# Kernel optimization log

Hardware: AMD Instinct MI355X
Metric: run time of the kernel (lower is better)

## Reference

```python
import jax, jax.numpy as jnp
import numpy as np

HEADS = 8
EPS = 1e-5
PW1 = (512, 8, 14, 14)   # (C, T, H, W), C = headsize1 * heads
PW2 = (512, 32, 7, 7)


def _ln(x, g, b):
    m = jnp.mean(x, axis=-1, keepdims=True)
    v = jnp.var(x, axis=-1, keepdims=True)
    return (x - m) * jax.lax.rsqrt(v + EPS) * g + b


def _mha(q, k, v):
    b, nq, c = q.shape
    nk = k.shape[1]
    hd = c // HEADS
    qh = q.reshape(b, nq, HEADS, hd).transpose(0, 2, 1, 3)  # [b,h,nq,hd]
    kh = k.reshape(b, nk, HEADS, hd).transpose(0, 2, 1, 3)
    vh = v.reshape(b, nk, HEADS, hd).transpose(0, 2, 1, 3)
    s = jnp.einsum('bhqd,bhkd->bhqk', qh, kh) * (hd ** -0.5)
    a = jax.nn.softmax(s, axis=-1)
    o = jnp.einsum('bhqk,bhkd->bhqd', a, vh)
    return o.transpose(0, 2, 1, 3).reshape(b, nq, c)


def _tok(x):
    b, c, t, h, w = x.shape
    return x.transpose(0, 2, 3, 4, 1).reshape(b, t * h * w, c)


def _detok(t, c, T, H, W):
    b = t.shape[0]
    return t.reshape(b, T, H, W, c).transpose(0, 4, 1, 2, 3)


def _out_head(y, w, bias, bn_g, bn_b):
    # 1x1x1 Conv3d + ReLU + BatchNorm3d (eval, running mean 0 / var 1)
    z = jnp.einsum('bcthw,oc->bothw', y, w) + bias[None, :, None, None, None]
    z = jax.nn.relu(z)
    z = z * jax.lax.rsqrt(jnp.float32(1.0 + EPS))
    return z * bn_g[None, :, None, None, None] + bn_b[None, :, None, None, None]


def reference(x1, x2, Wq1, bq1, Wk1, bk1, Wv1, bv1, ln1_g, ln1_b,
              Wq2, bq2, Wk2, bk2, Wv2, bv2, ln2_g, ln2_b,
              out1_w, out1_b, bn1_g, bn1_b, out2_w, out2_b, bn2_g, bn2_b):
    t1 = _tok(x1)  # [B, 1568, 512]
    t2 = _tok(x2)  # [B, 1568, 512]
    for i in range(3):  # three chained norm + cross-attn stages
        q1 = _ln(t1, ln1_g[i], ln1_b[i]) @ Wq1[i].T + bq1[i]
        k1 = t2 @ Wk1[i].T + bk1[i]
        v1 = t2 @ Wv1[i].T + bv1[i]
        q2 = _ln(t2, ln2_g[i], ln2_b[i]) @ Wq2[i].T + bq2[i]
        k2 = t1 @ Wk2[i].T + bk2[i]
        v2 = t1 @ Wv2[i].T + bv2[i]
        t1 = t1 + _mha(q1, k1, v1)
        t2 = t2 + _mha(q2, k2, v2)
    y1 = _detok(t1, *PW1)
    y2 = _detok(t2, *PW2)
    z1 = _out_head(y1, out1_w, out1_b, bn1_g, bn1_b)
    z2 = _out_head(y2, out2_w, out2_b, bn2_g, bn2_b)
    return (z1, z2)


def setup_inputs() -> dict:
    key = jax.random.key(0)
    ks = jax.random.split(key, 12)
    C = 512
    w = lambda k, shp: jax.random.normal(k, shp, jnp.float32) * 0.02
    return {
        'x1': jax.random.normal(ks[0], (4, C, 8, 14, 14), jnp.float32),
        'x2': jax.random.normal(ks[1], (4, C, 32, 7, 7), jnp.float32),
        'Wq1': w(ks[2], (3, C, C)), 'bq1': jnp.zeros((3, C), jnp.float32),
        'Wk1': w(ks[3], (3, C, C)), 'bk1': jnp.zeros((3, C), jnp.float32),
        'Wv1': w(ks[4], (3, C, C)), 'bv1': jnp.zeros((3, C), jnp.float32),
        'ln1_g': jnp.ones((3, C), jnp.float32), 'ln1_b': jnp.zeros((3, C), jnp.float32),
        'Wq2': w(ks[5], (3, C, C)), 'bq2': jnp.zeros((3, C), jnp.float32),
        'Wk2': w(ks[6], (3, C, C)), 'bk2': jnp.zeros((3, C), jnp.float32),
        'Wv2': w(ks[7], (3, C, C)), 'bv2': jnp.zeros((3, C), jnp.float32),
        'ln2_g': jnp.ones((3, C), jnp.float32), 'ln2_b': jnp.zeros((3, C), jnp.float32),
        'out1_w': w(ks[8], (C, C)), 'out1_b': jnp.zeros((C,), jnp.float32),
        'bn1_g': jnp.ones((C,), jnp.float32), 'bn1_b': jnp.zeros((C,), jnp.float32),
        'out2_w': w(ks[9], (C, C)), 'out2_b': jnp.zeros((C,), jnp.float32),
        'bn2_g': jnp.ones((C,), jnp.float32), 'bn2_b': jnp.zeros((C,), jnp.float32),
    }
```

## Files before the change

kernel.cpp:

```cpp
#include <hip/hip_runtime.h>

typedef __bf16 bf16_t;
typedef __bf16 bf16x8 __attribute__((ext_vector_type(8)));
typedef __bf16 bf16x4 __attribute__((ext_vector_type(4)));
typedef float f32x4 __attribute__((ext_vector_type(4)));
typedef float f32x16 __attribute__((ext_vector_type(16)));
typedef unsigned u32x4 __attribute__((ext_vector_type(4)));

#define NTOK 1568
#define CDIM 512
#define BATCH 4
#define MROWS (BATCH*NTOK)
#define RSQ1PEPS 0.9999950000374997f
#define CEXP 0.1803368801111204f

__device__ __forceinline__ float fexp2(float x) {
  float r;
  asm("v_exp_f32 %0, %1" : "=v"(r) : "v"(x));
  return r;
}

__device__ __forceinline__ void glds16(const bf16_t* src, bf16_t* dst) {
  __builtin_amdgcn_global_load_lds(
      (const __attribute__((address_space(1))) unsigned*)src,
      (__attribute__((address_space(3))) unsigned*)dst, 16, 0, 0);
}

struct CastArgs { const float* s[20]; };
__global__ __launch_bounds__(256) void cast_kernel(CastArgs ca, bf16_t* __restrict__ out) {
  int idx = blockIdx.x * 256 + threadIdx.x;
  int m = idx >> 16;
  const float4* sp = (const float4*)ca.s[m];
  float4 v = sp[idx & 65535];
  bf16x4 o;
  o[0] = (bf16_t)v.x; o[1] = (bf16_t)v.y; o[2] = (bf16_t)v.z; o[3] = (bf16_t)v.w;
  *(bf16x4*)(out + (size_t)idx * 4) = o;
}

struct TokArgs { const float* x[2]; float* tf[2]; bf16_t* tb[2]; };
__global__ __launch_bounds__(256) void tok_kernel(TokArgs ta) {
  __shared__ float tile[32][33];
  int z = blockIdx.z, sel = z >> 2, b = z & 3;
  int c0 = blockIdx.y * 32, s0 = blockIdx.x * 32;
  int tx = threadIdx.x, ty = threadIdx.y;
  const float* xp = ta.x[sel] + (size_t)b * CDIM * NTOK;
  for (int r = 0; r < 32; r += 8)
    tile[ty + r][tx] = xp[(size_t)(c0 + ty + r) * NTOK + s0 + tx];
  __syncthreads();
  float* tfp = ta.tf[sel] + (size_t)b * NTOK * CDIM;
  bf16_t* tbp = ta.tb[sel] + (size_t)b * NTOK * CDIM;
  for (int r = 0; r < 32; r += 8) {
    float v = tile[tx][ty + r];
    size_t idx = (size_t)(s0 + ty + r) * CDIM + c0 + tx;
    tfp[idx] = v;
    tbp[idx] = (bf16_t)v;
  }
}

__global__ __launch_bounds__(64) void ln_kernel(
    const float* __restrict__ t1, const float* __restrict__ t2,
    const float* __restrict__ g1, const float* __restrict__ b1,
    const float* __restrict__ g2, const float* __restrict__ b2,
    bf16_t* __restrict__ o1, bf16_t* __restrict__ o2) {
  int row = blockIdx.x;
  const float* t; const float* g; const float* bt; bf16_t* out;
  if (row < MROWS) { t = t1; g = g1; bt = b1; out = o1; }
  else { row -= MROWS; t = t2; g = g2; bt = b2; out = o2; }
  int l = threadIdx.x;
  const float* x = t + (size_t)row * CDIM;
  float4 v0 = ((const float4*)x)[l];
  float4 v1 = ((const float4*)x)[l + 64];
  float s = v0.x + v0.y + v0.z + v0.w + v1.x + v1.y + v1.z + v1.w;
  float sq = v0.x*v0.x + v0.y*v0.y + v0.z*v0.z + v0.w*v0.w
           + v1.x*v1.x + v1.y*v1.y + v1.z*v1.z + v1.w*v1.w;
  for (int m = 1; m < 64; m <<= 1) { s += __shfl_xor(s, m); sq += __shfl_xor(sq, m); }
  float mean = s * (1.f / 512.f);
  float var = sq * (1.f / 512.f) - mean * mean;
  float rs = rsqrtf(var + 1e-5f);
  float4 g0 = ((const float4*)g)[l], g1v = ((const float4*)g)[l + 64];
  float4 b0 = ((const float4*)bt)[l], b1v = ((const float4*)bt)[l + 64];
  bf16x4 o0, o1v;
  o0[0] = (bf16_t)((v0.x - mean) * rs * g0.x + b0.x);
  o0[1] = (bf16_t)((v0.y - mean) * rs * g0.y + b0.y);
  o0[2] = (bf16_t)((v0.z - mean) * rs * g0.z + b0.z);
  o0[3] = (bf16_t)((v0.w - mean) * rs * g0.w + b0.w);
  o1v[0] = (bf16_t)((v1.x - mean) * rs * g1v.x + b1v.x);
  o1v[1] = (bf16_t)((v1.y - mean) * rs * g1v.y + b1v.y);
  o1v[2] = (bf16_t)((v1.z - mean) * rs * g1v.z + b1v.z);
  o1v[3] = (bf16_t)((v1.w - mean) * rs * g1v.w + b1v.w);
  *(bf16x4*)(out + (size_t)row * CDIM + l * 4) = o0;
  *(bf16x4*)(out + (size_t)row * CDIM + 256 + l * 4) = o1v;
}

template<int MODE>
__device__ __forceinline__ void gemm_core(
    bf16_t (* __restrict__ As)[40], bf16_t (* __restrict__ Bs)[40],
    const bf16_t* __restrict__ A, const bf16_t* __restrict__ Bp,
    const float* __restrict__ bias, const float* __restrict__ bng,
    const float* __restrict__ bnb, bf16_t* __restrict__ outb,
    float* __restrict__ outf, int m0, int n0, int Nvalid, float scl) {
  int tid = threadIdx.x;
  int w = tid >> 6, l = tid & 63, lr = l & 15, kg = l >> 4;
  int wm = (w >> 1) * 64, wn = (w & 1) * 64;
  f32x4 acc[4][4];
  for (int i = 0; i < 4; i++)
    for (int j = 0; j < 4; j++)
      acc[i][j] = f32x4{0.f, 0.f, 0.f, 0.f};
  int srow = tid >> 1;
  int soff = (tid & 1) * 16;
  int brow = n0 + srow;
  if (MODE != 0 && brow >= Nvalid) brow = Nvalid - 1;
  const bf16_t* aq = A + (size_t)(m0 + srow) * CDIM + soff;
  const bf16_t* bq = Bp + (size_t)brow * CDIM + soff;
  for (int kk = 0; kk < 16; kk++) {
    __syncthreads();
    bf16x8 a0 = *(const bf16x8*)(aq);
    bf16x8 a1 = *(const bf16x8*)(aq + 8);
    bf16x8 b0 = *(const bf16x8*)(bq);
    bf16x8 b1 = *(const bf16x8*)(bq + 8);
    aq += 32; bq += 32;
    *(bf16x8*)&As[srow][soff] = a0;
    *(bf16x8*)&As[srow][soff + 8] = a1;
    *(bf16x8*)&Bs[srow][soff] = b0;
    *(bf16x8*)&Bs[srow][soff + 8] = b1;
    __syncthreads();
    bf16x8 af[4], bfr[4];
    for (int i = 0; i < 4; i++) af[i] = *(const bf16x8*)&As[wm + i * 16 + lr][kg * 8];
    for (int j = 0; j < 4; j++) bfr[j] = *(const bf16x8*)&Bs[wn + j * 16 + lr][kg * 8];
    for (int i = 0; i < 4; i++)
      for (int j = 0; j < 4; j++)
        acc[i][j] = __builtin_amdgcn_mfma_f32_16x16x32_bf16(af[i], bfr[j], acc[i][j], 0, 0, 0);
  }
  for (int i = 0; i < 4; i++)
    for (int j = 0; j < 4; j++) {
      int rbase = m0 + wm + i * 16 + kg * 4;
      int col = n0 + wn + j * 16 + lr;
      for (int r = 0; r < 4; r++) {
        int row = rbase + r;
        float v = acc[i][j][r];
        if (MODE == 0) {
          v = (v + bias[col]) * scl;
          outb[(size_t)row * CDIM + col] = (bf16_t)v;
        } else if (MODE == 1) {
          v += bias[row];
          v = v > 0.f ? v : 0.f;
          v *= RSQ1PEPS;
          v = v * bng[row] + bnb[row];
          if (col < Nvalid) outf[(size_t)row * NTOK + col] = v;
        } else {
          v += bias[row];
          if (col < Nvalid) outb[(size_t)row * NTOK + col] = (bf16_t)v;
        }
      }
    }
}

struct ProjArgs {
  const bf16_t* A0[4]; const bf16_t* W0[4]; const float* b0[4]; bf16_t* o0[4];
  float scl0[4];
  const bf16_t* W2[2]; const bf16_t* B2[2]; const float* b2[2]; bf16_t* o2[2];
};
__global__ __launch_bounds__(256) void proj_kernel(ProjArgs p) {
  __shared__ bf16_t As[128][40];
  __shared__ bf16_t Bs[128][40];
  int id = blockIdx.x;
  if (id < 784) {
    int set = id / 196, rem = id % 196;
    int n0 = (rem & 3) * 128, m0 = (rem >> 2) * 128;
    gemm_core<0>(As, Bs, p.A0[set], p.W0[set], p.b0[set], nullptr, nullptr,
                 p.o0[set], nullptr, m0, n0, 512, p.scl0[set]);
  } else {
    int j = id - 784;
    int unit = j / 52;
    int which = unit >> 2, bat = unit & 3;
    int rem = j % 52;
    int n0 = (rem % 13) * 128, m0 = (rem / 13) * 128;
    gemm_core<2>(As, Bs, p.W2[which], p.B2[which] + (size_t)bat * NTOK * CDIM,
                 p.b2[which], nullptr, nullptr,
                 p.o2[which] + (size_t)bat * CDIM * NTOK, nullptr, m0, n0, NTOK, 1.f);
  }
}

__global__ __launch_bounds__(256) void head_kernel(
    const bf16_t* __restrict__ W1, const bf16_t* __restrict__ W2,
    const bf16_t* __restrict__ t1b, const bf16_t* __restrict__ t2b,
    const float* __restrict__ b1, const float* __restrict__ b2,
    const float* __restrict__ bng1, const float* __restrict__ bnb1,
    const float* __restrict__ bng2, const float* __restrict__ bnb2,
    float* __restrict__ out) {
  __shared__ bf16_t As[128][40];
  __shared__ bf16_t Bs[128][40];
  int z = blockIdx.z;
  int which = z >> 2, bat = z & 3;
  const bf16_t* A = which ? W2 : W1;
  const bf16_t* Bp = (which ? t2b : t1b) + (size_t)bat * NTOK * CDIM;
  const float* bias = which ? b2 : b1;
  const float* bng = which ? bng2 : bng1;
  const float* bnb = which ? bnb2 : bnb1;
  float* outf = out + (size_t)which * BATCH * CDIM * NTOK + (size_t)bat * CDIM * NTOK;
  int m0 = blockIdx.y * 128, n0 = blockIdx.x * 128;
  gemm_core<1>(As, Bs, A, Bp, bias, bng, bnb, nullptr, outf, m0, n0, NTOK, 1.f);
}

__device__ __forceinline__ void build_frags(const float* p, bf16x8& Fa, bf16x8& Fb) {
  unsigned pk[8];
#pragma unroll
  for (int g = 0; g < 8; g++) {
    union { bf16_t hh[2]; unsigned u; } cv;
    cv.hh[0] = (bf16_t)p[2 * g];
    cv.hh[1] = (bf16_t)p[2 * g + 1];
    pk[g] = cv.u;
  }
  asm volatile("v_permlane32_swap_b32 %0, %1" : "+v"(pk[0]), "+v"(pk[2]));
  asm volatile("v_permlane32_swap_b32 %0, %1" : "+v"(pk[1]), "+v"(pk[3]));
  asm volatile("v_permlane32_swap_b32 %0, %1" : "+v"(pk[4]), "+v"(pk[6]));
  asm volatile("v_permlane32_swap_b32 %0, %1" : "+v"(pk[5]), "+v"(pk[7]));
  union { u32x4 u; bf16x8 bv; } A, B;
  A.u[0] = pk[0]; A.u[1] = pk[1]; A.u[2] = pk[2]; A.u[3] = pk[3];
  B.u[0] = pk[4]; B.u[1] = pk[5]; B.u[2] = pk[6]; B.u[3] = pk[7];
  Fa = A.bv; Fb = B.bv;
}

struct AttnArgs {
  const bf16_t* q[2]; const bf16_t* k[2]; const bf16_t* v[2];
  float* tf[2]; bf16_t* tb[2];
};

#define STAGE(TN, SL)                                                         \
  {                                                                           \
    int tnS_ = (TN); if (tnS_ > 48) tnS_ = 48;                                \
    glds16(kgl + (size_t)tnS_ * (32 * CDIM), &Ks[SL][wq8][0]);                \
    glds16(vgl + tnS_ * 32, &Vs[SL][wq16][0]);                                \
  }

#define QK(SL, SA)                                                            \
  {                                                                           \
    const bf16_t* kr_ = &Ks[SL][lo][0];                                       \
    __builtin_amdgcn_s_setprio(1);                                            \
    SA = __builtin_amdgcn_mfma_f32_32x32x16_bf16(                             \
        *(const bf16x8*)(kr_ + ((hi * 8) ^ sw3)), qf[0], z, 0, 0, 0);         \
    SA = __builtin_amdgcn_mfma_f32_32x32x16_bf16(                             \
        *(const bf16x8*)(kr_ + ((16 + hi * 8) ^ sw3)), qf[1], SA, 0, 0, 0);   \
    SA = __builtin_amdgcn_mfma_f32_32x32x16_bf16(                             \
        *(const bf16x8*)(kr_ + ((32 + hi * 8) ^ sw3)), qf[2], SA, 0, 0, 0);   \
    SA = __builtin_amdgcn_mfma_f32_32x32x16_bf16(                             \
        *(const bf16x8*)(kr_ + ((48 + hi * 8) ^ sw3)), qf[3], SA, 0, 0, 0);   \
    __builtin_amdgcn_s_setprio(0);                                            \
  }

#define FIN(SA, SL)                                                           \
  {                                                                           \
    float pa_[16];                                                            \
    _Pragma("unroll")                                                         \
    for (int r_ = 0; r_ < 16; r_++) pa_[r_] = fexp2(SA[r_]);                  \
    bf16x8 F0_, F1_;                                                          \
    build_frags(pa_, F0_, F1_);                                               \
    __builtin_amdgcn_s_setprio(1);                                            \
    ls = __builtin_amdgcn_mfma_f32_32x32x16_bf16(kone, F0_, ls, 0, 0, 0);     \
    ls = __builtin_amdgcn_mfma_f32_32x32x16_bf16(kone, F1_, ls, 0, 0, 0);     \
    ot0 = __builtin_amdgcn_mfma_f32_32x32x16_bf16(                            \
        *(const bf16x8*)(&Vs[SL][lo][(hi * 8) ^ sw2]), F0_, ot0, 0, 0, 0);    \
    ot0 = __builtin_amdgcn_mfma_f32_32x32x16_bf16(                            \
        *(const bf16x8*)(&Vs[SL][lo][(16 + hi * 8) ^ sw2]), F1_, ot0, 0, 0, 0);\
    ot1 = __builtin_amdgcn_mfma_f32_32x32x16_bf16(                            \
        *(const bf16x8*)(&Vs[SL][32 + lo][(hi * 8) ^ sw2]), F0_, ot1, 0, 0, 0);\
    ot1 = __builtin_amdgcn_mfma_f32_32x32x16_bf16(                            \
        *(const bf16x8*)(&Vs[SL][32 + lo][(16 + hi * 8) ^ sw2]), F1_, ot1, 0, 0, 0);\
    __builtin_amdgcn_s_setprio(0);                                            \
  }

#define PAIR(T, S0_, S1_, S2_, SS1, SS2)                                      \
  {                                                                           \
    STAGE((T) + 4, SS1);                                                      \
    STAGE((T) + 5, SS2);                                                      \
    QK(S1_, saB);                                                             \
    FIN(saA, S0_);                                                            \
    QK(S2_, saA);                                                             \
    FIN(saB, S1_);                                                            \
    asm volatile("s_waitcnt vmcnt(2)" ::: "memory");                          \
    __builtin_amdgcn_s_barrier();                                             \
  }

__global__ __launch_bounds__(256) void attn_kernel(AttnArgs aa) {
  __shared__ alignas(16) bf16_t Ks[6][32][64];
  __shared__ alignas(16) bf16_t Vs[6][64][32];
  int id = blockIdx.x;
  int xcd = id & 7, sl = id >> 3;
  int g = xcd + ((sl / 13) << 3);
  int qt = sl % 13;
  int ss = g >> 5, b = (g >> 3) & 3, h = g & 7;
  const bf16_t* qg = aa.q[ss];
  const bf16_t* kgp = aa.k[ss];
  const bf16_t* vtg = aa.v[ss];
  float* tf = aa.tf[ss];
  bf16_t* tb = aa.tb[ss];
  int tid = threadIdx.x, w = tid >> 6, l = tid & 63;
  int lo = l & 31, hi = l >> 5;
  int wq8 = w * 8, wq16 = w * 16;
  int sw3 = (lo & 7) << 3;
  int sw2 = ((lo >> 1) & 3) << 3;
  const size_t kbase = ((size_t)b * NTOK) * CDIM + h * 64;
  const size_t vbase = ((size_t)b * CDIM + h * 64) * NTOK;

  int q0 = qt * 128 + w * 32;
  int qrow = q0 + lo;
  int qr = qrow < NTOK ? qrow : NTOK - 1;
  const bf16_t* qp = qg + kbase + (size_t)qr * CDIM + hi * 8;
  bf16x8 qf[4];
  qf[0] = *(const bf16x8*)(qp);
  qf[1] = *(const bf16x8*)(qp + 16);
  qf[2] = *(const bf16x8*)(qp + 32);
  qf[3] = *(const bf16x8*)(qp + 48);
  asm volatile("" : "+v"(qf[0]), "+v"(qf[1]), "+v"(qf[2]), "+v"(qf[3]));
  asm volatile("s_waitcnt vmcnt(0)" ::: "memory");

  const bf16_t* kgl = kgp + kbase + (size_t)(wq8 + (l >> 3)) * CDIM
                      + (((l & 7) ^ ((l >> 3) & 7)) << 3);
  const bf16_t* vgl = vtg + vbase + (size_t)(wq16 + (l >> 2)) * NTOK
                      + (((l & 3) ^ ((l >> 3) & 3)) << 3);

  bf16x8 kone;
#pragma unroll
  for (int j = 0; j < 8; j++) kone[j] = (bf16_t)1.0f;

  f32x16 ot0, ot1, ls, z, saA, saB;
#pragma unroll
  for (int r = 0; r < 16; r++) { ot0[r] = 0.f; ot1[r] = 0.f; ls[r] = 0.f; z[r] = 0.f; }

  STAGE(0, 0);
  STAGE(1, 1);
  STAGE(2, 2);
  STAGE(3, 3);
  asm volatile("s_waitcnt vmcnt(2)" ::: "memory");
  __builtin_amdgcn_s_barrier();
  QK(0, saA);

  for (int t = 0; t <= 42; t += 6) {
    PAIR(t + 0, 0, 1, 2, 4, 5);
    PAIR(t + 2, 2, 3, 4, 0, 1);
    PAIR(t + 4, 4, 5, 0, 2, 3);
  }
  FIN(saA, 0);
  asm volatile("s_waitcnt vmcnt(0)" ::: "memory");

  if (qrow < NTOK) {
    float inv = 1.f / ls[0];
    float* tfp = tf + ((size_t)b * NTOK + qrow) * CDIM + h * 64 + hi * 4;
    bf16_t* tbp = tb + ((size_t)b * NTOK + qrow) * CDIM + h * 64 + hi * 4;
#pragma unroll
    for (int db = 0; db < 2; db++) {
#pragma unroll
      for (int gq = 0; gq < 4; gq++) {
        int doff = db * 32 + gq * 8;
        float4 old = *(float4*)(tfp + doff);
        float4 nv;
        float a0 = (db ? ot1[gq * 4 + 0] : ot0[gq * 4 + 0]) * inv;
        float a1 = (db ? ot1[gq * 4 + 1] : ot0[gq * 4 + 1]) * inv;
        float a2 = (db ? ot1[gq * 4 + 2] : ot0[gq * 4 + 2]) * inv;
        float a3 = (db ? ot1[gq * 4 + 3] : ot0[gq * 4 + 3]) * inv;
        nv.x = old.x + a0; nv.y = old.y + a1; nv.z = old.z + a2; nv.w = old.w + a3;
        *(float4*)(tfp + doff) = nv;
        bf16x4 ob;
        ob[0] = (bf16_t)nv.x; ob[1] = (bf16_t)nv.y;
        ob[2] = (bf16_t)nv.z; ob[3] = (bf16_t)nv.w;
        *(bf16x4*)(tbp + doff) = ob;
      }
    }
  }
}

extern "C" void kernel_launch(void* const* d_in, const int* in_sizes, int n_in,
                              void* d_out, int out_size, void* d_ws, size_t ws_size,
                              hipStream_t stream) {
  (void)in_sizes; (void)n_in; (void)out_size; (void)ws_size;
  const float* x1 = (const float*)d_in[0];
  const float* x2 = (const float*)d_in[1];
  const float* Wq1 = (const float*)d_in[2];
  const float* bq1 = (const float*)d_in[3];
  const float* Wk1 = (const float*)d_in[4];
  const float* bk1 = (const float*)d_in[5];
  const float* Wv1 = (const float*)d_in[6];
  const float* bv1 = (const float*)d_in[7];
  const float* ln1_g = (const float*)d_in[8];
  const float* ln1_b = (const float*)d_in[9];
  const float* Wq2 = (const float*)d_in[10];
  const float* bq2 = (const float*)d_in[11];
  const float* Wk2 = (const float*)d_in[12];
  const float* bk2 = (const float*)d_in[13];
  const float* Wv2 = (const float*)d_in[14];
  const float* bv2 = (const float*)d_in[15];
  const float* ln2_g = (const float*)d_in[16];
  const float* ln2_b = (const float*)d_in[17];
  const float* out1_w = (const float*)d_in[18];
  const float* out1_b = (const float*)d_in[19];
  const float* bn1_g = (const float*)d_in[20];
  const float* bn1_b = (const float*)d_in[21];
  const float* out2_w = (const float*)d_in[22];
  const float* out2_b = (const float*)d_in[23];
  const float* bn2_g = (const float*)d_in[24];
  const float* bn2_b = (const float*)d_in[25];

  const size_t WMAT = 512 * 512;
  char* ws = (char*)d_ws;
  bf16_t* wb = (bf16_t*)ws;
  size_t off = 20 * WMAT * sizeof(bf16_t);
  float* t1f = (float*)(ws + off); off += (size_t)MROWS * CDIM * 4;
  float* t2f = (float*)(ws + off); off += (size_t)MROWS * CDIM * 4;
  bf16_t* t1b = (bf16_t*)(ws + off); off += (size_t)MROWS * CDIM * 2;
  bf16_t* t2b = (bf16_t*)(ws + off); off += (size_t)MROWS * CDIM * 2;
  bf16_t* l1b = (bf16_t*)(ws + off); off += (size_t)MROWS * CDIM * 2;
  bf16_t* l2b = (bf16_t*)(ws + off); off += (size_t)MROWS * CDIM * 2;
  bf16_t* q1b = (bf16_t*)(ws + off); off += (size_t)MROWS * CDIM * 2;
  bf16_t* k1b = (bf16_t*)(ws + off); off += (size_t)MROWS * CDIM * 2;
  bf16_t* v1b = (bf16_t*)(ws + off); off += (size_t)MROWS * CDIM * 2;
  bf16_t* q2b = (bf16_t*)(ws + off); off += (size_t)MROWS * CDIM * 2;
  bf16_t* k2b = (bf16_t*)(ws + off); off += (size_t)MROWS * CDIM * 2;
  bf16_t* v2b = (bf16_t*)(ws + off); off += (size_t)MROWS * CDIM * 2;

  CastArgs ca;
  for (int i = 0; i < 3; i++) {
    ca.s[0 + i] = Wq1 + (size_t)i * WMAT;
    ca.s[3 + i] = Wk1 + (size_t)i * WMAT;
    ca.s[6 + i] = Wv1 + (size_t)i * WMAT;
    ca.s[9 + i] = Wq2 + (size_t)i * WMAT;
    ca.s[12 + i] = Wk2 + (size_t)i * WMAT;
    ca.s[15 + i] = Wv2 + (size_t)i * WMAT;
  }
  ca.s[18] = out1_w;
  ca.s[19] = out2_w;
  cast_kernel<<<5120, 256, 0, stream>>>(ca, wb);

  TokArgs ta;
  ta.x[0] = x1; ta.x[1] = x2;
  ta.tf[0] = t1f; ta.tf[1] = t2f;
  ta.tb[0] = t1b; ta.tb[1] = t2b;
  tok_kernel<<<dim3(49, 16, 8), dim3(32, 8), 0, stream>>>(ta);

  AttnArgs aa;
  aa.q[0] = q1b; aa.q[1] = q2b;
  aa.k[0] = k1b; aa.k[1] = k2b;
  aa.v[0] = v1b; aa.v[1] = v2b;
  aa.tf[0] = t1f; aa.tf[1] = t2f;
  aa.tb[0] = t1b; aa.tb[1] = t2b;

  for (int i = 0; i < 3; i++) {
    ln_kernel<<<2 * MROWS, 64, 0, stream>>>(t1f, t2f,
        ln1_g + i * 512, ln1_b + i * 512, ln2_g + i * 512, ln2_b + i * 512,
        l1b, l2b);
    ProjArgs pa;
    pa.A0[0] = l1b; pa.W0[0] = wb + (0 + i) * WMAT; pa.b0[0] = bq1 + i * 512; pa.o0[0] = q1b;
    pa.A0[1] = t2b; pa.W0[1] = wb + (3 + i) * WMAT; pa.b0[1] = bk1 + i * 512; pa.o0[1] = k1b;
    pa.A0[2] = l2b; pa.W0[2] = wb + (9 + i) * WMAT; pa.b0[2] = bq2 + i * 512; pa.o0[2] = q2b;
    pa.A0[3] = t1b; pa.W0[3] = wb + (12 + i) * WMAT; pa.b0[3] = bk2 + i * 512; pa.o0[3] = k2b;
    pa.scl0[0] = CEXP; pa.scl0[1] = 1.f; pa.scl0[2] = CEXP; pa.scl0[3] = 1.f;
    pa.W2[0] = wb + (6 + i) * WMAT; pa.B2[0] = t2b; pa.b2[0] = bv1 + i * 512; pa.o2[0] = v1b;
    pa.W2[1] = wb + (15 + i) * WMAT; pa.B2[1] = t1b; pa.b2[1] = bv2 + i * 512; pa.o2[1] = v2b;
    proj_kernel<<<1200, 256, 0, stream>>>(pa);
    attn_kernel<<<832, 256, 0, stream>>>(aa);
  }

  float* out = (float*)d_out;
  head_kernel<<<dim3(13, 4, 8), 256, 0, stream>>>(
      wb + 18 * WMAT, wb + 19 * WMAT, t1b, t2b,
      out1_b, out2_b, bn1_g, bn1_b, bn2_g, bn2_b, out);
}
```

Baseline: 394.7 us.

## Double-buffer GEMM tiles with direct global-to-LDS loads and XOR swizzle

```diff
diff --git a/kernel.cpp b/kernel.cpp
--- a/kernel.cpp
+++ b/kernel.cpp
@@ -94,7 +94,7 @@
 
 template<int MODE>
 __device__ __forceinline__ void gemm_core(
-    bf16_t (* __restrict__ As)[40], bf16_t (* __restrict__ Bs)[40],
+    bf16_t (* __restrict__ As)[128][32], bf16_t (* __restrict__ Bs)[128][32],
     const bf16_t* __restrict__ A, const bf16_t* __restrict__ Bp,
     const float* __restrict__ bias, const float* __restrict__ bng,
     const float* __restrict__ bnb, bf16_t* __restrict__ outb,
@@ -106,31 +106,47 @@
   for (int i = 0; i < 4; i++)
     for (int j = 0; j < 4; j++)
       acc[i][j] = f32x4{0.f, 0.f, 0.f, 0.f};
-  int srow = tid >> 1;
-  int soff = (tid & 1) * 16;
-  int brow = n0 + srow;
-  if (MODE != 0 && brow >= Nvalid) brow = Nvalid - 1;
-  const bf16_t* aq = A + (size_t)(m0 + srow) * CDIM + soff;
-  const bf16_t* bq = Bp + (size_t)brow * CDIM + soff;
+
+  int srow = w * 16 + (l >> 2);
+  int scol = ((l & 3) ^ ((l >> 3) & 3)) << 3;
+  const bf16_t* aq0 = A + (size_t)(m0 + srow) * CDIM + scol;
+  const bf16_t* aq1 = aq0 + (size_t)64 * CDIM;
+  int br0 = n0 + srow, br1 = n0 + srow + 64;
+  if (MODE != 0) {
+    if (br0 > Nvalid - 1) br0 = Nvalid - 1;
+    if (br1 > Nvalid - 1) br1 = Nvalid - 1;
+  }
+  const bf16_t* bq0 = Bp + (size_t)br0 * CDIM + scol;
+  const bf16_t* bq1 = Bp + (size_t)br1 * CDIM + scol;
+  int swr = ((lr >> 1) & 3) << 3;
+  int wq = w * 16;
+
+  glds16(aq0, &As[0][wq][0]);
+  glds16(aq1, &As[0][64 + wq][0]);
+  glds16(bq0, &Bs[0][wq][0]);
+  glds16(bq1, &Bs[0][64 + wq][0]);
+  __syncthreads();
+
   for (int kk = 0; kk < 16; kk++) {
-    __syncthreads();
-    bf16x8 a0 = *(const bf16x8*)(aq);
-    bf16x8 a1 = *(const bf16x8*)(aq + 8);
-    bf16x8 b0 = *(const bf16x8*)(bq);
-    bf16x8 b1 = *(const bf16x8*)(bq + 8);
-    aq += 32; bq += 32;
-    *(bf16x8*)&As[srow][soff] = a0;
-    *(bf16x8*)&As[srow][soff + 8] = a1;
-    *(bf16x8*)&Bs[srow][soff] = b0;
-    *(bf16x8*)&Bs[srow][soff + 8] = b1;
-    __syncthreads();
+    int bu = kk & 1;
+    if (kk < 15) {
+      int ko = (kk + 1) * 32;
+      glds16(aq0 + ko, &As[bu ^ 1][wq][0]);
+      glds16(aq1 + ko, &As[bu ^ 1][64 + wq][0]);
+      glds16(bq0 + ko, &Bs[bu ^ 1][wq][0]);
+      glds16(bq1 + ko, &Bs[bu ^ 1][64 + wq][0]);
+    }
     bf16x8 af[4], bfr[4];
-    for (int i = 0; i < 4; i++) af[i] = *(const bf16x8*)&As[wm + i * 16 + lr][kg * 8];
-    for (int j = 0; j < 4; j++) bfr[j] = *(const bf16x8*)&Bs[wn + j * 16 + lr][kg * 8];
+    for (int i = 0; i < 4; i++)
+      af[i] = *(const bf16x8*)&As[bu][wm + i * 16 + lr][(kg * 8) ^ swr];
+    for (int j = 0; j < 4; j++)
+      bfr[j] = *(const bf16x8*)&Bs[bu][wn + j * 16 + lr][(kg * 8) ^ swr];
     for (int i = 0; i < 4; i++)
       for (int j = 0; j < 4; j++)
         acc[i][j] = __builtin_amdgcn_mfma_f32_16x16x32_bf16(af[i], bfr[j], acc[i][j], 0, 0, 0);
-  }
+    __syncthreads();
+  }
+
   for (int i = 0; i < 4; i++)
     for (int j = 0; j < 4; j++) {
       int rbase = m0 + wm + i * 16 + kg * 4;
@@ -161,8 +177,8 @@
   const bf16_t* W2[2]; const bf16_t* B2[2]; const float* b2[2]; bf16_t* o2[2];
 };
 __global__ __launch_bounds__(256) void proj_kernel(ProjArgs p) {
-  __shared__ bf16_t As[128][40];
-  __shared__ bf16_t Bs[128][40];
+  __shared__ alignas(16) bf16_t As[2][128][32];
+  __shared__ alignas(16) bf16_t Bs[2][128][32];
   int id = blockIdx.x;
   if (id < 784) {
     int set = id / 196, rem = id % 196;
@@ -188,8 +204,8 @@
     const float* __restrict__ bng1, const float* __restrict__ bnb1,
     const float* __restrict__ bng2, const float* __restrict__ bnb2,
     float* __restrict__ out) {
-  __shared__ bf16_t As[128][40];
-  __shared__ bf16_t Bs[128][40];
+  __shared__ alignas(16) bf16_t As[2][128][32];
+  __shared__ alignas(16) bf16_t Bs[2][128][32];
   int z = blockIdx.z;
   int which = z >> 2, bat = z & 3;
   const bf16_t* A = which ? W2 : W1;
```

New measurement: 390.6 us. About the same (-1.0%).
